# Kernel tuning notes

Measured on AMD Instinct MI355X. Metric: run time of the kernel, lower is better.

The kernel has to match this reference:

```python
import jax, jax.numpy as jnp
import numpy as np

B, S, D, H = 4, 2048, 512, 8
DK = D // H  # 64


def setup_inputs() -> dict:
    key = jax.random.key(0)
    ks = jax.random.split(key, 7)
    return {
        "q": jax.random.normal(ks[0], (B, S, D), dtype=jnp.float32),
        "k": jax.random.normal(ks[1], (B, S, D), dtype=jnp.float32),
        "v": jax.random.normal(ks[2], (B, S, D), dtype=jnp.float32),
        # per-head query projection weights (also used for k and v, replicating
        # the source's bug where q_linear projects all three inputs)
        "Wq": jax.random.normal(ks[3], (H, DK, D), dtype=jnp.float32) * (1.0 / np.sqrt(D)),
        "bq": jax.random.normal(ks[4], (H, DK), dtype=jnp.float32) * 0.02,
        "Wout": jax.random.normal(ks[5], (D, H * DK), dtype=jnp.float32) * (1.0 / np.sqrt(D)),
        "bout": jax.random.normal(ks[6], (D,), dtype=jnp.float32) * 0.02,
    }


def reference(q, k, v, Wq, bq, Wout, bout):
    # Per-head projections, batched over heads. NOTE: the original module
    # (buggy but faithful) applies the SAME q_linear to q, k and v.
    scale = 1.0 / jnp.sqrt(jnp.asarray(Wq.shape[1], dtype=q.dtype))
    qh = jnp.einsum("bsd,hed->bhse", q, Wq) + bq[:, None, :]  # [B,H,S,DK]
    kh = jnp.einsum("bsd,hed->bhse", k, Wq) + bq[:, None, :]
    vh = jnp.einsum("bsd,hed->bhse", v, Wq) + bq[:, None, :]
    scores = jnp.einsum("bhqe,bhke->bhqk", qh, kh) * scale  # [B,H,S,S]
    weights = jax.nn.softmax(scores, axis=-1)
    heads = jnp.einsum("bhqk,bhke->bhqe", weights, vh)  # [B,H,S,DK]
    # concat heads along feature dim (head-major order matches torch.cat)
    concat = heads.transpose(0, 2, 1, 3).reshape(q.shape[0], q.shape[1], -1)
    return concat @ Wout.T + bout
```

## Files before the change

kernel.cpp:

```cpp
#include <hip/hip_runtime.h>

#define BB 4
#define SS 2048
#define DD 512
#define HH 8
#define DKK 64
#define HDK 512

typedef __attribute__((ext_vector_type(4))) float f32x4;
typedef __attribute__((ext_vector_type(8))) __bf16 bf16x8;
typedef __attribute__((ext_vector_type(4))) __bf16 bf16x4;

#define MFMA16(a, b, c) __builtin_amdgcn_mfma_f32_16x16x32_bf16((a), (b), (c), 0, 0, 0)

#define GLOAD_LDS16(gptr, lptr)                                                    \
    __builtin_amdgcn_global_load_lds(                                              \
        (const __attribute__((address_space(1))) void*)(gptr),                     \
        (__attribute__((address_space(3))) void*)(lptr), 16, 0, 0)

__device__ inline bf16x8 cvt48(const f32x4 f0, const f32x4 f1) {
    bf16x8 w;
    w[0] = (__bf16)f0[0]; w[1] = (__bf16)f0[1]; w[2] = (__bf16)f0[2]; w[3] = (__bf16)f0[3];
    w[4] = (__bf16)f1[0]; w[5] = (__bf16)f1[1]; w[6] = (__bf16)f1[2]; w[7] = (__bf16)f1[3];
    return w;
}

__global__ __launch_bounds__(256) void proj_kernel(
    const float* __restrict__ q, const float* __restrict__ k, const float* __restrict__ v,
    const float* __restrict__ Wq, const float* __restrict__ bq,
    __bf16* __restrict__ qh, __bf16* __restrict__ kh, __bf16* __restrict__ vt)
{
    const int z  = blockIdx.z;
    const float* X = (z == 0) ? q : (z == 1) ? k : v;
    const int m0 = blockIdx.x * 128;
    const int n0 = blockIdx.y * 128;

    __shared__ __align__(16) float As0[128 * 32], Bs0[128 * 32];
    __shared__ __align__(16) float As1[128 * 32], Bs1[128 * 32];

    const int t    = threadIdx.x;
    const int lane = t & 63, wid = t >> 6;
    const int lo   = lane & 15, hi = lane >> 4;
    const int wm   = wid >> 1, wn = wid & 1;

    const int lrow = lane >> 3;
    const int lchk = ((lane & 7) ^ lrow) << 4;
    const char* aSrc = (const char*)(X  + (size_t)(m0 + 32 * wid + lrow) * DD) + lchk;
    const char* bSrc = (const char*)(Wq + (size_t)(n0 + 32 * wid + lrow) * DD) + lchk;

    f32x4 acc[4][4] = {};

    auto stage = [&](float* Ab, float* Bb, int tt) {
#pragma unroll
        for (int i = 0; i < 4; ++i) {
            GLOAD_LDS16(aSrc + (size_t)i * (8 * DD * 4) + (size_t)tt * 128,
                        (char*)Ab + (32 * wid + 8 * i) * 128);
            GLOAD_LDS16(bSrc + (size_t)i * (8 * DD * 4) + (size_t)tt * 128,
                        (char*)Bb + (32 * wid + 8 * i) * 128);
        }
    };
    auto compute = [&](const float* Ab, const float* Bb) {
        bf16x8 a[4], b[4];
#pragma unroll
        for (int mi = 0; mi < 4; ++mi) {
            const int ar = wm * 64 + mi * 16 + lo;
            const int sw = (ar & 7) << 4;
            f32x4 f0 = *reinterpret_cast<const f32x4*>((const char*)Ab + ar * 128 + ((32 * hi) ^ sw));
            f32x4 f1 = *reinterpret_cast<const f32x4*>((const char*)Ab + ar * 128 + ((32 * hi + 16) ^ sw));
            a[mi] = cvt48(f0, f1);
        }
#pragma unroll
        for (int ni = 0; ni < 4; ++ni) {
            const int br = wn * 64 + ni * 16 + lo;
            const int sw = (br & 7) << 4;
            f32x4 f0 = *reinterpret_cast<const f32x4*>((const char*)Bb + br * 128 + ((32 * hi) ^ sw));
            f32x4 f1 = *reinterpret_cast<const f32x4*>((const char*)Bb + br * 128 + ((32 * hi + 16) ^ sw));
            b[ni] = cvt48(f0, f1);
        }
        __builtin_amdgcn_s_setprio(1);
#pragma unroll
        for (int mi = 0; mi < 4; ++mi)
#pragma unroll
            for (int ni = 0; ni < 4; ++ni)
                acc[mi][ni] = MFMA16(a[mi], b[ni], acc[mi][ni]);
        __builtin_amdgcn_s_setprio(0);
    };

    float *Ac = As0, *Bc = Bs0, *An = As1, *Bn = Bs1;
    stage(Ac, Bc, 0);
    __syncthreads();
    for (int tt = 0; tt < 16; ++tt) {
        if (tt < 15) stage(An, Bn, tt + 1);
        compute(Ac, Bc);
        __syncthreads();
        float* tmp;
        tmp = Ac; Ac = An; An = tmp;
        tmp = Bc; Bc = Bn; Bn = tmp;
    }

#pragma unroll
    for (int mi = 0; mi < 4; ++mi) {
#pragma unroll
        for (int ni = 0; ni < 4; ++ni) {
            const int n = n0 + wn * 64 + ni * 16 + lo;
            const float bias = bq[n];
            const int h_ = n >> 6, e_ = n & 63;
#pragma unroll
            for (int r = 0; r < 4; ++r) {
                const int m = m0 + wm * 64 + mi * 16 + hi * 4 + r;
                const float val = acc[mi][ni][r] + bias;
                const int b_ = m >> 11, s_ = m & (SS - 1);
                const size_t bh = (size_t)(b_ * HH + h_);
                if (z == 0)
                    qh[(bh * SS + s_) * DKK + e_] = (__bf16)val;
                else if (z == 1)
                    kh[(bh * SS + s_) * DKK + e_] = (__bf16)val;
                else
                    vt[(bh * DKK + e_) * SS + s_] = (__bf16)val;
            }
        }
    }
}

__global__ __launch_bounds__(256) void attn_kernel(
    const __bf16* __restrict__ qh, const __bf16* __restrict__ kh,
    const __bf16* __restrict__ vt, __bf16* __restrict__ concat)
{
    const int q0 = blockIdx.x * 64;
    const int bh = blockIdx.y;
    const int b_ = bh >> 3, h_ = bh & 7;
    const size_t base = (size_t)bh * SS * DKK;
    const __bf16* qhp = qh + base;
    const __bf16* khp = kh + base;
    const __bf16* vtp = vt + base;

    const int t    = threadIdx.x;
    const int lane = t & 63, wid = t >> 6;
    const int lo   = lane & 15, hi = lane >> 4;

    __shared__ __align__(16) __bf16 Ks[128 * 64];
    __shared__ __align__(16) __bf16 Vts[64 * 128];
    __shared__ __align__(16) __bf16 Ps[4][16][136];

    char* KsB  = (char*)Ks;
    char* VtsB = (char*)Vts;
    char* PsB  = (char*)Ps + wid * (16 * 272) + lo * 272;

    const int kr = lane >> 3;
    const int kc = (lane & 7) << 4;
    const char* kSrc = (const char*)khp + (size_t)(32 * wid + kr) * 128 + kc;
    const int   kDst = (32 * wid + kr) * 128 + (kc ^ (kr << 4));
    const int vr = lane >> 4;
    const int vc = (lane & 15) << 4;
    const char* vSrc = (const char*)vtp + (size_t)(16 * wid + vr) * (SS * 2) + vc;

    bf16x8 qf[2];
#pragma unroll
    for (int kk = 0; kk < 2; ++kk)
        qf[kk] = *reinterpret_cast<const bf16x8*>(
            &qhp[(size_t)(q0 + 16 * wid + lo) * DKK + 32 * kk + 8 * hi]);

    const int rsw = (lo & 7) << 4;

    f32x4 acc[4] = {};
    float m_run = -INFINITY, l_run = 0.f;

    for (int tile = 0; tile < SS / 128; ++tile) {
        bf16x8 kreg[4], vreg[4];
#pragma unroll
        for (int j = 0; j < 4; ++j) {
            kreg[j] = *reinterpret_cast<const bf16x8*>(kSrc + j * (8 * 128));
            vreg[j] = *reinterpret_cast<const bf16x8*>(vSrc + (size_t)j * (4 * SS * 2));
        }
        kSrc += 128 * 128;
        vSrc += 128 * 2;

        __syncthreads();
#pragma unroll
        for (int j = 0; j < 4; ++j) {
            *reinterpret_cast<bf16x8*>(KsB + kDst + j * (8 * 128)) = kreg[j];
            const int vrow = 16 * wid + 4 * j + vr;
            *reinterpret_cast<bf16x8*>(VtsB + vrow * 256 + (vc ^ ((vrow & 7) << 4))) = vreg[j];
        }
        __syncthreads();

        f32x4 sc[8] = {};
        __builtin_amdgcn_s_setprio(1);
#pragma unroll
        for (int kk = 0; kk < 2; ++kk) {
            const int cb = (kk * 64 + 16 * hi) ^ rsw;
#pragma unroll
            for (int f = 0; f < 8; ++f) {
                bf16x8 kf = *reinterpret_cast<const bf16x8*>(KsB + (16 * f + lo) * 128 + cb);
                sc[f] = MFMA16(kf, qf[kk], sc[f]);
            }
        }
        __builtin_amdgcn_s_setprio(0);

        {
            float mx = sc[0][0];
#pragma unroll
            for (int f = 0; f < 8; ++f)
#pragma unroll
                for (int r = 0; r < 4; ++r)
                    mx = fmaxf(mx, sc[f][r]);
            mx = fmaxf(mx, __shfl_xor(mx, 16));
            mx = fmaxf(mx, __shfl_xor(mx, 32));
            const float mxs = mx * 0.125f;
            if (!__all(mxs <= m_run + 8.0f)) {
                const float mnew = fmaxf(m_run, mxs);
                const float scl  = __expf(m_run - mnew);
                l_run *= scl;
#pragma unroll
                for (int f = 0; f < 4; ++f)
                    acc[f] *= scl;
                m_run = mnew;
            }
            float rs = 0.f;
#pragma unroll
            for (int f = 0; f < 8; ++f) {
                bf16x4 pk;
#pragma unroll
                for (int r = 0; r < 4; ++r) {
                    const float e = __expf(fmaf(sc[f][r], 0.125f, -m_run));
                    rs += e;
                    pk[r] = (__bf16)e;
                }
                *reinterpret_cast<bf16x4*>(PsB + 32 * f + 8 * hi) = pk;
            }
            rs += __shfl_xor(rs, 16);
            rs += __shfl_xor(rs, 32);
            l_run += rs;
        }

        __builtin_amdgcn_s_setprio(1);
#pragma unroll
        for (int kk = 0; kk < 4; ++kk) {
            bf16x8 pb = *reinterpret_cast<const bf16x8*>(PsB + 64 * kk + 16 * hi);
            const int cb = (kk * 64 + 16 * hi) ^ rsw;
#pragma unroll
            for (int f = 0; f < 4; ++f) {
                bf16x8 vf = *reinterpret_cast<const bf16x8*>(VtsB + (16 * f + lo) * 256 + cb);
                acc[f] = MFMA16(vf, pb, acc[f]);
            }
        }
        __builtin_amdgcn_s_setprio(0);
    }

    {
        const float inv = 1.0f / l_run;
        const int qrow = q0 + 16 * wid + lo;
        const size_t ob = ((size_t)b_ * SS + qrow) * HDK + h_ * DKK;
#pragma unroll
        for (int f = 0; f < 4; ++f) {
            bf16x4 o;
#pragma unroll
            for (int r = 0; r < 4; ++r)
                o[r] = (__bf16)(acc[f][r] * inv);
            *reinterpret_cast<bf16x4*>(&concat[ob + 16 * f + 4 * hi]) = o;
        }
    }
}

__global__ __launch_bounds__(256) void outproj_kernel(
    const __bf16* __restrict__ concat, const float* __restrict__ Wout,
    const float* __restrict__ bout, float* __restrict__ out)
{
    const int m0 = blockIdx.x * 64;
    const int n0 = blockIdx.y * 128;

    __shared__ __align__(16) __bf16 As0[64 * 32], As1[64 * 32];
    __shared__ __align__(16) float  Bs0[128 * 32], Bs1[128 * 32];

    const int t    = threadIdx.x;
    const int lane = t & 63, wid = t >> 6;
    const int lo   = lane & 15, hi = lane >> 4;
    const int wm   = wid >> 1, wn = wid & 1;

    const int ar4  = lane >> 2;
    const int achk = ((lane & 3) ^ (ar4 & 3)) << 4;
    const char* aSrc = (const char*)(concat + (size_t)(m0 + 16 * wid + ar4) * HDK) + achk;
    const int br8  = lane >> 3;
    const int bchk = ((lane & 7) ^ br8) << 4;
    const char* bSrc = (const char*)(Wout + (size_t)(n0 + 32 * wid + br8) * HDK) + bchk;

    f32x4 acc[2][4] = {};

    auto stage = [&](__bf16* Ab, float* Bb, int tt) {
        GLOAD_LDS16(aSrc + (size_t)tt * 64, (char*)Ab + (16 * wid) * 64);
#pragma unroll
        for (int i = 0; i < 4; ++i)
            GLOAD_LDS16(bSrc + (size_t)i * (8 * HDK * 4) + (size_t)tt * 128,
                        (char*)Bb + (32 * wid + 8 * i) * 128);
    };
    auto compute = [&](const __bf16* Ab, const float* Bb) {
        bf16x8 a[2], b[4];
#pragma unroll
        for (int mi = 0; mi < 2; ++mi) {
            const int ar = wm * 32 + mi * 16 + lo;
            a[mi] = *reinterpret_cast<const bf16x8*>(
                (const char*)Ab + ar * 64 + ((16 * hi) ^ ((ar & 3) << 4)));
        }
#pragma unroll
        for (int ni = 0; ni < 4; ++ni) {
            const int br = wn * 64 + ni * 16 + lo;
            const int sw = (br & 7) << 4;
            f32x4 f0 = *reinterpret_cast<const f32x4*>((const char*)Bb + br * 128 + ((32 * hi) ^ sw));
            f32x4 f1 = *reinterpret_cast<const f32x4*>((const char*)Bb + br * 128 + ((32 * hi + 16) ^ sw));
            b[ni] = cvt48(f0, f1);
        }
        __builtin_amdgcn_s_setprio(1);
#pragma unroll
        for (int mi = 0; mi < 2; ++mi)
#pragma unroll
            for (int ni = 0; ni < 4; ++ni)
                acc[mi][ni] = MFMA16(a[mi], b[ni], acc[mi][ni]);
        __builtin_amdgcn_s_setprio(0);
    };

    __bf16 *Ac = As0, *An = As1;
    float  *Bc = Bs0, *Bn = Bs1;
    stage(Ac, Bc, 0);
    __syncthreads();
    for (int tt = 0; tt < 16; ++tt) {
        if (tt < 15) stage(An, Bn, tt + 1);
        compute(Ac, Bc);
        __syncthreads();
        __bf16* ta = Ac; Ac = An; An = ta;
        float*  tb = Bc; Bc = Bn; Bn = tb;
    }

#pragma unroll
    for (int mi = 0; mi < 2; ++mi) {
#pragma unroll
        for (int ni = 0; ni < 4; ++ni) {
            const int n = n0 + wn * 64 + ni * 16 + lo;
            const float bias = bout[n];
#pragma unroll
            for (int r = 0; r < 4; ++r) {
                const int m = m0 + wm * 32 + mi * 16 + hi * 4 + r;
                out[(size_t)m * DD + n] = acc[mi][ni][r] + bias;
            }
        }
    }
}

extern "C" void kernel_launch(void* const* d_in, const int* in_sizes, int n_in,
                              void* d_out, int out_size, void* d_ws, size_t ws_size,
                              hipStream_t stream)
{
    (void)in_sizes; (void)n_in; (void)out_size; (void)ws_size;
    const float* q    = (const float*)d_in[0];
    const float* k    = (const float*)d_in[1];
    const float* v    = (const float*)d_in[2];
    const float* Wq   = (const float*)d_in[3];
    const float* bq   = (const float*)d_in[4];
    const float* Wout = (const float*)d_in[5];
    const float* bout = (const float*)d_in[6];
    float* out = (float*)d_out;

    char* ws = (char*)d_ws;
    __bf16* qh = (__bf16*)(ws);
    __bf16* kh = (__bf16*)(ws + (8u << 20));
    __bf16* vt = (__bf16*)(ws + (16u << 20));
    __bf16* cc = (__bf16*)(ws + (24u << 20));

    proj_kernel<<<dim3(BB * SS / 128, HDK / 128, 3), 256, 0, stream>>>(q, k, v, Wq, bq, qh, kh, vt);
    attn_kernel<<<dim3(SS / 64, BB * HH), 256, 0, stream>>>(qh, kh, vt, cc);
    outproj_kernel<<<dim3(BB * SS / 64, DD / 128), 256, 0, stream>>>(cc, Wout, bout, out);
}
```

Baseline: 228.0 us.

## Pipeline GEMM staging with vmcnt waits and shrink attention tiles to 32x64

The two GEMM kernels now keep two global_load_lds stages in flight. They use explicit vmcnt/lgkmcnt waits with raw barriers instead of full __syncthreads, which should hide load latency better. The attention kernel moves to 128-thread blocks covering 32 queries and walks KV in 64-wide tiles, giving twice as many blocks and less LDS per block. It also drops the lazy-rescale threshold and always rescales, and removes the setprio hints. This trades more blocks and occupancy for more loop iterations and extra rescale work per tile.

```diff
diff --git a/kernel.cpp b/kernel.cpp
--- a/kernel.cpp
+++ b/kernel.cpp
@@ -17,6 +17,11 @@
     __builtin_amdgcn_global_load_lds(                                              \
         (const __attribute__((address_space(1))) void*)(gptr),                     \
         (__attribute__((address_space(3))) void*)(lptr), 16, 0, 0)
+
+#define WAITCNT_VM(N) do { asm volatile("s_waitcnt vmcnt(" #N ")" ::: "memory");   \
+                           __builtin_amdgcn_sched_barrier(0); } while (0)
+#define WAITCNT_LGKM0() do { asm volatile("s_waitcnt lgkmcnt(0)" ::: "memory");    \
+                             __builtin_amdgcn_sched_barrier(0); } while (0)
 
 __device__ inline bf16x8 cvt48(const f32x4 f0, const f32x4 f1) {
     bf16x8 w;
@@ -88,15 +93,21 @@
 
     float *Ac = As0, *Bc = Bs0, *An = As1, *Bn = Bs1;
     stage(Ac, Bc, 0);
-    __syncthreads();
-    for (int tt = 0; tt < 16; ++tt) {
-        if (tt < 15) stage(An, Bn, tt + 1);
+    stage(An, Bn, 1);
+    for (int tt = 0; tt < 15; ++tt) {
+        WAITCNT_VM(8);
+        __builtin_amdgcn_s_barrier();
         compute(Ac, Bc);
-        __syncthreads();
+        WAITCNT_LGKM0();
+        __builtin_amdgcn_s_barrier();
+        if (tt < 14) stage(Ac, Bc, tt + 2);
         float* tmp;
         tmp = Ac; Ac = An; An = tmp;
         tmp = Bc; Bc = Bn; Bn = tmp;
     }
+    WAITCNT_VM(0);
+    __builtin_amdgcn_s_barrier();
+    compute(Ac, Bc);
 
 #pragma unroll
     for (int mi = 0; mi < 4; ++mi) {
@@ -122,11 +133,11 @@
     }
 }
 
-__global__ __launch_bounds__(256) void attn_kernel(
+__global__ __launch_bounds__(128) void attn_kernel(
     const __bf16* __restrict__ qh, const __bf16* __restrict__ kh,
     const __bf16* __restrict__ vt, __bf16* __restrict__ concat)
 {
-    const int q0 = blockIdx.x * 64;
+    const int q0 = blockIdx.x * 32;
     const int bh = blockIdx.y;
     const int b_ = bh >> 3, h_ = bh & 7;
     const size_t base = (size_t)bh * SS * DKK;
@@ -138,21 +149,17 @@
     const int lane = t & 63, wid = t >> 6;
     const int lo   = lane & 15, hi = lane >> 4;
 
-    __shared__ __align__(16) __bf16 Ks[128 * 64];
-    __shared__ __align__(16) __bf16 Vts[64 * 128];
-    __shared__ __align__(16) __bf16 Ps[4][16][136];
+    __shared__ __align__(16) __bf16 Ks[64 * 64];
+    __shared__ __align__(16) __bf16 Vts[64 * 64];
+    __shared__ __align__(16) __bf16 Ps[2][16][72];
 
     char* KsB  = (char*)Ks;
     char* VtsB = (char*)Vts;
-    char* PsB  = (char*)Ps + wid * (16 * 272) + lo * 272;
-
-    const int kr = lane >> 3;
-    const int kc = (lane & 7) << 4;
-    const char* kSrc = (const char*)khp + (size_t)(32 * wid + kr) * 128 + kc;
-    const int   kDst = (32 * wid + kr) * 128 + (kc ^ (kr << 4));
-    const int vr = lane >> 4;
-    const int vc = (lane & 15) << 4;
-    const char* vSrc = (const char*)vtp + (size_t)(16 * wid + vr) * (SS * 2) + vc;
+
+    const int sr   = lane >> 3;
+    const int gcb  = (lane & 7) << 4;
+    const int scb  = gcb ^ (sr << 4);
+    const int srow = 32 * wid + sr;
 
     bf16x8 qf[2];
 #pragma unroll
@@ -160,91 +167,85 @@
         qf[kk] = *reinterpret_cast<const bf16x8*>(
             &qhp[(size_t)(q0 + 16 * wid + lo) * DKK + 32 * kk + 8 * hi]);
 
-    const int rsw = (lo & 7) << 4;
-
     f32x4 acc[4] = {};
     float m_run = -INFINITY, l_run = 0.f;
 
-    for (int tile = 0; tile < SS / 128; ++tile) {
+    for (int kv0 = 0; kv0 < SS; kv0 += 64) {
         bf16x8 kreg[4], vreg[4];
 #pragma unroll
         for (int j = 0; j < 4; ++j) {
-            kreg[j] = *reinterpret_cast<const bf16x8*>(kSrc + j * (8 * 128));
-            vreg[j] = *reinterpret_cast<const bf16x8*>(vSrc + (size_t)j * (4 * SS * 2));
-        }
-        kSrc += 128 * 128;
-        vSrc += 128 * 2;
+            kreg[j] = *reinterpret_cast<const bf16x8*>(
+                (const char*)&khp[(size_t)(kv0 + srow + 8 * j) * DKK] + gcb);
+            vreg[j] = *reinterpret_cast<const bf16x8*>(
+                (const char*)&vtp[(size_t)(srow + 8 * j) * SS + kv0] + gcb);
+        }
 
         __syncthreads();
 #pragma unroll
         for (int j = 0; j < 4; ++j) {
-            *reinterpret_cast<bf16x8*>(KsB + kDst + j * (8 * 128)) = kreg[j];
-            const int vrow = 16 * wid + 4 * j + vr;
-            *reinterpret_cast<bf16x8*>(VtsB + vrow * 256 + (vc ^ ((vrow & 7) << 4))) = vreg[j];
+            *reinterpret_cast<bf16x8*>(KsB  + (srow + 8 * j) * 128 + scb) = kreg[j];
+            *reinterpret_cast<bf16x8*>(VtsB + (srow + 8 * j) * 128 + scb) = vreg[j];
         }
         __syncthreads();
 
-        f32x4 sc[8] = {};
-        __builtin_amdgcn_s_setprio(1);
+        f32x4 sc[4] = {};
 #pragma unroll
         for (int kk = 0; kk < 2; ++kk) {
-            const int cb = (kk * 64 + 16 * hi) ^ rsw;
-#pragma unroll
-            for (int f = 0; f < 8; ++f) {
-                bf16x8 kf = *reinterpret_cast<const bf16x8*>(KsB + (16 * f + lo) * 128 + cb);
-                sc[f] = MFMA16(kf, qf[kk], sc[f]);
-            }
-        }
-        __builtin_amdgcn_s_setprio(0);
+            bf16x8 kf[4];
+#pragma unroll
+            for (int f = 0; f < 4; ++f) {
+                const int row = 16 * f + lo;
+                const int cb  = (64 * kk + 16 * hi) ^ ((row & 7) << 4);
+                kf[f] = *reinterpret_cast<const bf16x8*>(KsB + row * 128 + cb);
+            }
+#pragma unroll
+            for (int f = 0; f < 4; ++f)
+                sc[f] = MFMA16(kf[f], qf[kk], sc[f]);
+        }
 
         {
-            float mx = sc[0][0];
-#pragma unroll
-            for (int f = 0; f < 8; ++f)
+            float mx = -1e30f;
+#pragma unroll
+            for (int f = 0; f < 4; ++f)
 #pragma unroll
                 for (int r = 0; r < 4; ++r)
                     mx = fmaxf(mx, sc[f][r]);
             mx = fmaxf(mx, __shfl_xor(mx, 16));
             mx = fmaxf(mx, __shfl_xor(mx, 32));
-            const float mxs = mx * 0.125f;
-            if (!__all(mxs <= m_run + 8.0f)) {
-                const float mnew = fmaxf(m_run, mxs);
-                const float scl  = __expf(m_run - mnew);
-                l_run *= scl;
-#pragma unroll
-                for (int f = 0; f < 4; ++f)
-                    acc[f] *= scl;
-                m_run = mnew;
-            }
+            const float mnew = fmaxf(m_run, mx * 0.125f);
+            const float scl  = __expf(m_run - mnew);
             float rs = 0.f;
 #pragma unroll
-            for (int f = 0; f < 8; ++f) {
+            for (int f = 0; f < 4; ++f) {
                 bf16x4 pk;
 #pragma unroll
                 for (int r = 0; r < 4; ++r) {
-                    const float e = __expf(fmaf(sc[f][r], 0.125f, -m_run));
+                    const float e = __expf(fmaf(sc[f][r], 0.125f, -mnew));
                     rs += e;
                     pk[r] = (__bf16)e;
                 }
-                *reinterpret_cast<bf16x4*>(PsB + 32 * f + 8 * hi) = pk;
+                *reinterpret_cast<bf16x4*>(&Ps[wid][lo][16 * f + 4 * hi]) = pk;
             }
             rs += __shfl_xor(rs, 16);
             rs += __shfl_xor(rs, 32);
-            l_run += rs;
-        }
-
-        __builtin_amdgcn_s_setprio(1);
-#pragma unroll
-        for (int kk = 0; kk < 4; ++kk) {
-            bf16x8 pb = *reinterpret_cast<const bf16x8*>(PsB + 64 * kk + 16 * hi);
-            const int cb = (kk * 64 + 16 * hi) ^ rsw;
+            l_run = l_run * scl + rs;
+            m_run = mnew;
+#pragma unroll
+            for (int f = 0; f < 4; ++f)
+                acc[f] *= scl;
+        }
+
+#pragma unroll
+        for (int kk = 0; kk < 2; ++kk) {
+            bf16x8 pb = *reinterpret_cast<const bf16x8*>(&Ps[wid][lo][32 * kk + 8 * hi]);
 #pragma unroll
             for (int f = 0; f < 4; ++f) {
-                bf16x8 vf = *reinterpret_cast<const bf16x8*>(VtsB + (16 * f + lo) * 256 + cb);
+                const int row = 16 * f + lo;
+                const int cb  = (64 * kk + 16 * hi) ^ ((row & 7) << 4);
+                bf16x8 vf = *reinterpret_cast<const bf16x8*>(VtsB + row * 128 + cb);
                 acc[f] = MFMA16(vf, pb, acc[f]);
             }
         }
-        __builtin_amdgcn_s_setprio(0);
     }
 
     {
@@ -321,14 +322,20 @@
     __bf16 *Ac = As0, *An = As1;
     float  *Bc = Bs0, *Bn = Bs1;
     stage(Ac, Bc, 0);
-    __syncthreads();
-    for (int tt = 0; tt < 16; ++tt) {
-        if (tt < 15) stage(An, Bn, tt + 1);
+    stage(An, Bn, 1);
+    for (int tt = 0; tt < 15; ++tt) {
+        WAITCNT_VM(5);
+        __builtin_amdgcn_s_barrier();
         compute(Ac, Bc);
-        __syncthreads();
+        WAITCNT_LGKM0();
+        __builtin_amdgcn_s_barrier();
+        if (tt < 14) stage(Ac, Bc, tt + 2);
         __bf16* ta = Ac; Ac = An; An = ta;
         float*  tb = Bc; Bc = Bn; Bn = tb;
     }
+    WAITCNT_VM(0);
+    __builtin_amdgcn_s_barrier();
+    compute(Ac, Bc);
 
 #pragma unroll
     for (int mi = 0; mi < 2; ++mi) {
@@ -366,6 +373,6 @@
     __bf16* cc = (__bf16*)(ws + (24u << 20));
 
     proj_kernel<<<dim3(BB * SS / 128, HDK / 128, 3), 256, 0, stream>>>(q, k, v, Wq, bq, qh, kh, vt);
-    attn_kernel<<<dim3(SS / 64, BB * HH), 256, 0, stream>>>(qh, kh, vt, cc);
+    attn_kernel<<<dim3(SS / 32, BB * HH), 128, 0, stream>>>(qh, kh, vt, cc);
     outproj_kernel<<<dim3(BB * SS / 64, DD / 128), 256, 0, stream>>>(cc, Wout, bout, out);
 }
```

Measured after the change: 254.2 us. 11.5% more time.
